# Kernel tuning notes

Measured on AMD Instinct MI355X. Metric: run time of the kernel, lower is better.

The kernel has to match this reference:

```python
import jax, jax.numpy as jnp
import numpy as np

DN = ('NCHW', 'OIHW', 'NCHW')


def setup_inputs() -> dict:
    key = jax.random.key(0)
    k1, k2, k3, k4 = jax.random.split(key, 4)
    B, C, H, W = 8, 64, 128, 416
    depth = jax.random.uniform(k1, (B, H, W), dtype=jnp.float32) * 10.0 + 1.0
    feat = jax.random.normal(k2, (B, C, H, W), dtype=jnp.float32)
    w1 = jax.random.normal(k3, (64, C, 3, 3), dtype=jnp.float32) * 0.05
    w2 = jax.random.normal(k4, (144, 64, 1, 1), dtype=jnp.float32) * 0.05
    return {"depth": depth, "feat": feat, "w1": w1, "w2": w2}


def reference(depth, feat, w1, w2):
    B, H, W = depth.shape
    S = 4  # 2 ** scale, scale=2
    # mask predictor: conv3x3 (no bias) -> relu -> conv1x1 (no bias)
    h = jax.lax.conv_general_dilated(feat, w1, (1, 1), ((1, 1), (1, 1)), dimension_numbers=DN)
    h = jax.nn.relu(h)
    mask = jax.lax.conv_general_dilated(h, w2, (1, 1), ((0, 0), (0, 0)), dimension_numbers=DN)
    # [B, 144, H, W] -> [B, 9, S, S, H, W], softmax over the 9 neighbor taps
    mask = mask.reshape(B, 9, S, S, H, W)
    mask = jax.nn.softmax(mask, axis=1)
    # unfold(depth, 3x3, pad=1): 9 shifted views, row-major (ky, kx) like torch
    pad = jnp.pad(depth, ((0, 0), (1, 1), (1, 1)))
    patches = jnp.stack([pad[:, ky:ky + H, kx:kx + W]
                         for ky in range(3) for kx in range(3)], axis=1)  # [B,9,H,W]
    up = jnp.sum(mask * patches[:, :, None, None], axis=1)  # [B,S,S,H,W]
    # pixel-shuffle: permute(0,3,1,4,2) -> [B,H,S,W,S] -> [B,S*H,S*W]
    out = up.transpose(0, 3, 1, 4, 2).reshape(B, S * H, S * W)
    return out
```

## Files before the change

kernel.cpp:

```cpp
#include <hip/hip_runtime.h>


using frag_ab = __attribute__((ext_vector_type(8))) short;
using frag_cd = __attribute__((ext_vector_type(4))) float;
typedef __attribute__((ext_vector_type(8))) unsigned short ushort8;

static __device__ __forceinline__ unsigned short f2bf(float f) {
    unsigned u = __builtin_bit_cast(unsigned, f);
    u += 0x7fff + ((u >> 16) & 1);
    return (unsigned short)(u >> 16);
}

__global__ void prep(const float* __restrict__ w1, const float* __restrict__ w2,
                     unsigned short* __restrict__ w1bf, unsigned short* __restrict__ w2bf,
                     unsigned short* __restrict__ nhwc, int do_pad) {
    int i = blockIdx.x * 256 + threadIdx.x;
    if (i < 36864) {
        int j = i & 7, oc = (i >> 3) & 63, g = i >> 9;
        int q = g & 3, kh = (g >> 2) & 1, tap = g >> 3;
        int ic = kh * 32 + q * 8 + j;
        w1bf[i] = f2bf(w1[(oc * 64 + ic) * 9 + (tap / 3) * 3 + (tap % 3)]);
    }
    if (i < 9216) {
        int j = i & 7, ch = (i >> 3) % 144, g = (i >> 3) / 144;
        int q = g & 3, kh = g >> 2;
        w2bf[i] = f2bf(w2[ch * 64 + (kh * 32 + q * 8 + j)]);
    }
    if (do_pad && i < 69888) {
        int b = i / 8736, rem = i - b * 8736;
        int pos = rem >> 3, pack = rem & 7;
        int row, w;
        if (pos < 836) { row = (pos < 418) ? 0 : 129; w = (pos < 418) ? pos : pos - 418; }
        else           { int t = pos - 836; row = 1 + (t >> 1); w = (t & 1) ? 417 : 0; }
        ushort8 z = {0, 0, 0, 0, 0, 0, 0, 0};
        *(ushort8*)&nhwc[(((size_t)b * 130 + row) * 418 + w) * 64 + pack * 8] = z;
    }
}

__global__ __launch_bounds__(256, 8) void nchw_to_nhwc(const float* __restrict__ feat,
                                                       unsigned short* __restrict__ nhwc) {
    __shared__ unsigned short sT[32 * 64];
    const int b = blockIdx.z, h = blockIdx.y, w0 = blockIdx.x * 32;
    const int tid = threadIdx.x;
    const int c = tid >> 2, j = tid & 3;
    const float* src = feat + (((size_t)b * 64 + c) * 128 + h) * 416 + w0 + j * 8;
    float4 v0 = *(const float4*)src;
    float4 v1 = *(const float4*)(src + 4);
    sT[(j * 8 + 0) * 64 + c] = f2bf(v0.x);
    sT[(j * 8 + 1) * 64 + c] = f2bf(v0.y);
    sT[(j * 8 + 2) * 64 + c] = f2bf(v0.z);
    sT[(j * 8 + 3) * 64 + c] = f2bf(v0.w);
    sT[(j * 8 + 4) * 64 + c] = f2bf(v1.x);
    sT[(j * 8 + 5) * 64 + c] = f2bf(v1.y);
    sT[(j * 8 + 6) * 64 + c] = f2bf(v1.z);
    sT[(j * 8 + 7) * 64 + c] = f2bf(v1.w);
    __syncthreads();
    const int w = tid >> 3, pack = tid & 7;
    ushort8 val = *(ushort8*)&sT[w * 64 + pack * 8];
    *(ushort8*)&nhwc[(((size_t)b * 130 + h + 1) * 418 + (w0 + w + 1)) * 64 + pack * 8] = val;
}

__global__ __launch_bounds__(256, 4) void convex_up_mfma2(
    const float* __restrict__ depth, const unsigned short* __restrict__ nhwc,
    const unsigned short* __restrict__ w1bf, const unsigned short* __restrict__ w2bf,
    float* __restrict__ out)
{
    constexpr int H = 128, W = 416, OW = 1664;
    constexpr int RS = 418 * 64;

    __shared__ __align__(16) unsigned short sF[1440 * 8];
    __shared__ float sD[180];

    const int tid  = threadIdx.x;
    const int wv   = tid >> 6;
    const int lane = tid & 63;
    const int q    = lane >> 4;
    const int ln   = lane & 15;
    const int bw = blockIdx.x, bh = blockIdx.y, b = blockIdx.z;
    const int h0 = bh * 8, w0 = bw * 16;

    if (tid < 180) {
        int lr = tid / 18, lc = tid % 18;
        int gh = h0 - 1 + lr, gw = w0 - 1 + lc;
        float v = 0.f;
        if ((unsigned)gh < (unsigned)H && (unsigned)gw < (unsigned)W)
            v = depth[((size_t)b * H + gh) * W + gw];
        sD[tid] = v;
    }

    const unsigned short* gbase = nhwc + ((size_t)(b * 130 + h0) * 418 + w0) * 64;
    #pragma unroll
    for (int k = 0; k < 6; ++k) {
        int i = wv + 4 * k;
        int c = i * 64 + lane;
        if (c < 1440) {
            int r = c / 144, m = c - r * 144;
            int col = m >> 3, iccs = m & 7;
            int icc = iccs ^ (col & 7);
            const unsigned short* g = gbase + (size_t)r * RS + col * 64 + icc * 8;
            __builtin_amdgcn_global_load_lds((const __attribute__((address_space(1))) void*)g,
                                             (__attribute__((address_space(3))) void*)&sF[c * 8],
                                             16, 0, 0);
        }
    }
    __syncthreads();

    frag_cd acc1[2][4];
    #pragma unroll
    for (int mt = 0; mt < 2; ++mt)
        #pragma unroll
        for (int nt = 0; nt < 4; ++nt) acc1[mt][nt] = frag_cd{0.f, 0.f, 0.f, 0.f};

    #pragma unroll
    for (int tap = 0; tap < 9; ++tap) {
        const int ky = tap / 3, kx = tap % 3;
        #pragma unroll
        for (int kh = 0; kh < 2; ++kh) {
            frag_ab a[2];
            #pragma unroll
            for (int mt = 0; mt < 2; ++mt) {
                int r = 2 * wv + mt + ky, col = ln + kx;
                int slot = (r * 18 + col) * 8 + ((kh * 4 + q) ^ (col & 7));
                a[mt] = *(const frag_ab*)&sF[slot * 8];
            }
            frag_ab bf[4];
            #pragma unroll
            for (int nt = 0; nt < 4; ++nt)
                bf[nt] = *(const frag_ab*)&w1bf[(size_t)((tap * 2 + kh) * 4 + q) * 512 + (nt * 16 + ln) * 8];
            #pragma unroll
            for (int mt = 0; mt < 2; ++mt)
                #pragma unroll
                for (int nt = 0; nt < 4; ++nt)
                    acc1[mt][nt] = __builtin_amdgcn_mfma_f32_16x16x32_bf16(a[mt], bf[nt], acc1[mt][nt], 0, 0, 0);
        }
    }

    __syncthreads();

    unsigned short* sH = sF + wv * 2304;
    #pragma unroll
    for (int mt = 0; mt < 2; ++mt)
        #pragma unroll
        for (int nt = 0; nt < 4; ++nt)
            #pragma unroll
            for (int r = 0; r < 4; ++r)
                sH[(mt * 16 + q * 4 + r) * 72 + nt * 16 + ln] = f2bf(fmaxf(acc1[mt][nt][r], 0.f));

    frag_cd acc2[2][9];
    #pragma unroll
    for (int mt = 0; mt < 2; ++mt)
        #pragma unroll
        for (int nt = 0; nt < 9; ++nt) acc2[mt][nt] = frag_cd{0.f, 0.f, 0.f, 0.f};

    #pragma unroll
    for (int kh = 0; kh < 2; ++kh) {
        frag_ab a2[2];
        #pragma unroll
        for (int mt = 0; mt < 2; ++mt)
            a2[mt] = *(const frag_ab*)&sH[(mt * 16 + ln) * 72 + kh * 32 + q * 8];
        #pragma unroll
        for (int nt = 0; nt < 9; ++nt) {
            frag_ab b2 = *(const frag_ab*)&w2bf[(size_t)((kh * 4 + q) * 144 + nt * 16 + ln) * 8];
            acc2[0][nt] = __builtin_amdgcn_mfma_f32_16x16x32_bf16(a2[0], b2, acc2[0][nt], 0, 0, 0);
            acc2[1][nt] = __builtin_amdgcn_mfma_f32_16x16x32_bf16(a2[1], b2, acc2[1][nt], 0, 0, 0);
        }
    }

    float* sOutw = (float*)sH;
    #pragma unroll
    for (int mt = 0; mt < 2; ++mt) {
        const int prow = 2 * wv + mt;
        #pragma unroll
        for (int r = 0; r < 4; ++r) {
            const int pcol = q * 4 + r;
            float lg[9];
            #pragma unroll
            for (int t = 0; t < 9; ++t) lg[t] = acc2[mt][t][r];
            float mx = lg[0];
            #pragma unroll
            for (int t = 1; t < 9; ++t) mx = fmaxf(mx, lg[t]);
            float sum = 0.f, up = 0.f;
            #pragma unroll
            for (int t = 0; t < 9; ++t) {
                float e = __expf(lg[t] - mx);
                sum += e;
                up  += e * sD[(prow + t / 3) * 18 + (pcol + t % 3)];
            }
            sOutw[(mt * 16 + pcol) * 17 + ln] = up / sum;
        }
    }
    float* outb = out + (size_t)b * 512 * OW + (size_t)(h0 + 2 * wv) * 4 * OW + w0 * 4;
    const int row_o = lane >> 3;
    const int mt_o  = row_o >> 2, sy_o = row_o & 3;
    #pragma unroll
    for (int v = 0; v < 2; ++v) {
        float4 o;
        #pragma unroll
        for (int e = 0; e < 4; ++e) {
            int j = (lane & 7) * 8 + v * 4 + e;
            o[e] = sOutw[(mt_o * 16 + (j >> 2)) * 17 + sy_o * 4 + (j & 3)];
        }
        *(float4*)&outb[(size_t)row_o * OW + (lane & 7) * 8 + v * 4] = o;
    }
}

__global__ __launch_bounds__(256, 3) void convex_up_mfma_fb(
    const float* __restrict__ depth, const float* __restrict__ feat,
    const unsigned short* __restrict__ w1bf, const unsigned short* __restrict__ w2bf,
    float* __restrict__ out)
{
    constexpr int H = 128, W = 416, OW = 1664;
    __shared__ unsigned short sF[8 * 10 * 18 * 8];
    __shared__ unsigned short sH[4][32 * 72];
    __shared__ float sD[10 * 18];
    const int tid = threadIdx.x, wv = tid >> 6, lane = tid & 63;
    const int q = lane >> 4, ln = lane & 15;
    const int bw = blockIdx.x, bh = blockIdx.y, b = blockIdx.z;
    const int h0 = bh * 8, w0 = bw * 16;
    if (tid < 180) {
        int lr = tid / 18, lc = tid % 18;
        int gh = h0 - 1 + lr, gw = w0 - 1 + lc;
        float v = 0.f;
        if ((unsigned)gh < (unsigned)H && (unsigned)gw < (unsigned)W)
            v = depth[((size_t)b * H + gh) * W + gw];
        sD[tid] = v;
    }
    for (int idx = tid; idx < 11520; idx += 256) {
        int ic = idx / 180, rem = idx - ic * 180;
        int lr = rem / 18, lc = rem - lr * 18;
        int gh = h0 - 1 + lr, gw = w0 - 1 + lc;
        float v = 0.f;
        if ((unsigned)gh < (unsigned)H && (unsigned)gw < (unsigned)W)
            v = feat[(((size_t)b * 64 + ic) * H + gh) * W + gw];
        sF[(((ic >> 3) * 10 + lr) * 18 + lc) * 8 + (ic & 7)] = f2bf(v);
    }
    __syncthreads();
    frag_cd acc1[2][4];
    for (int mt = 0; mt < 2; ++mt) for (int nt = 0; nt < 4; ++nt) acc1[mt][nt] = frag_cd{0.f,0.f,0.f,0.f};
    #pragma unroll
    for (int tap = 0; tap < 9; ++tap) {
        const int ky = tap / 3, kx = tap % 3;
        #pragma unroll
        for (int kh = 0; kh < 2; ++kh) {
            frag_ab a[2];
            #pragma unroll
            for (int mt = 0; mt < 2; ++mt)
                a[mt] = *(const frag_ab*)&sF[(((kh * 4 + q) * 10 + 2 * wv + mt + ky) * 18 + ln + kx) * 8];
            frag_ab bf[4];
            #pragma unroll
            for (int nt = 0; nt < 4; ++nt)
                bf[nt] = *(const frag_ab*)&w1bf[(size_t)((tap * 2 + kh) * 4 + q) * 512 + (nt * 16 + ln) * 8];
            #pragma unroll
            for (int mt = 0; mt < 2; ++mt)
                #pragma unroll
                for (int nt = 0; nt < 4; ++nt)
                    acc1[mt][nt] = __builtin_amdgcn_mfma_f32_16x16x32_bf16(a[mt], bf[nt], acc1[mt][nt], 0, 0, 0);
        }
    }
    #pragma unroll
    for (int mt = 0; mt < 2; ++mt)
        #pragma unroll
        for (int nt = 0; nt < 4; ++nt)
            #pragma unroll
            for (int r = 0; r < 4; ++r)
                sH[wv][(mt * 16 + q * 4 + r) * 72 + nt * 16 + ln] = f2bf(fmaxf(acc1[mt][nt][r], 0.f));
    frag_cd acc2[2][9];
    for (int mt = 0; mt < 2; ++mt) for (int nt = 0; nt < 9; ++nt) acc2[mt][nt] = frag_cd{0.f,0.f,0.f,0.f};
    #pragma unroll
    for (int kh = 0; kh < 2; ++kh) {
        frag_ab a2[2];
        #pragma unroll
        for (int mt = 0; mt < 2; ++mt)
            a2[mt] = *(const frag_ab*)&sH[wv][(mt * 16 + ln) * 72 + kh * 32 + q * 8];
        #pragma unroll
        for (int nt = 0; nt < 9; ++nt) {
            frag_ab b2 = *(const frag_ab*)&w2bf[(size_t)((kh * 4 + q) * 144 + nt * 16 + ln) * 8];
            acc2[0][nt] = __builtin_amdgcn_mfma_f32_16x16x32_bf16(a2[0], b2, acc2[0][nt], 0, 0, 0);
            acc2[1][nt] = __builtin_amdgcn_mfma_f32_16x16x32_bf16(a2[1], b2, acc2[1][nt], 0, 0, 0);
        }
    }
    float* sOutw = (float*)&sH[wv][0];
    #pragma unroll
    for (int mt = 0; mt < 2; ++mt) {
        const int prow = 2 * wv + mt;
        #pragma unroll
        for (int r = 0; r < 4; ++r) {
            const int pcol = q * 4 + r;
            float lg[9];
            #pragma unroll
            for (int t = 0; t < 9; ++t) lg[t] = acc2[mt][t][r];
            float mx = lg[0];
            #pragma unroll
            for (int t = 1; t < 9; ++t) mx = fmaxf(mx, lg[t]);
            float sum = 0.f, up = 0.f;
            #pragma unroll
            for (int t = 0; t < 9; ++t) {
                float e = __expf(lg[t] - mx);
                sum += e; up += e * sD[(prow + t / 3) * 18 + (pcol + t % 3)];
            }
            sOutw[(mt * 16 + pcol) * 17 + ln] = up / sum;
        }
    }
    float* outb = out + (size_t)b * 512 * OW + (size_t)(h0 + 2 * wv) * 4 * OW + w0 * 4;
    const int row_o = lane >> 3, mt_o = row_o >> 2, sy_o = row_o & 3;
    #pragma unroll
    for (int v = 0; v < 2; ++v) {
        float4 o;
        #pragma unroll
        for (int e = 0; e < 4; ++e) {
            int j = (lane & 7) * 8 + v * 4 + e;
            o[e] = sOutw[(mt_o * 16 + (j >> 2)) * 17 + sy_o * 4 + (j & 3)];
        }
        *(float4*)&outb[(size_t)row_o * OW + (lane & 7) * 8 + v * 4] = o;
    }
}

extern "C" void kernel_launch(void* const* d_in, const int* in_sizes, int n_in,
                              void* d_out, int out_size, void* d_ws, size_t ws_size,
                              hipStream_t stream) {
    const float* depth = (const float*)d_in[0];
    const float* feat  = (const float*)d_in[1];
    const float* w1    = (const float*)d_in[2];
    const float* w2    = (const float*)d_in[3];
    float* out = (float*)d_out;

    const size_t NHWC_USHORTS = (size_t)8 * 130 * 418 * 64;
    const size_t NEED = NHWC_USHORTS * 2 + (36864 + 9216) * 2;

    if (ws_size >= NEED) {
        unsigned short* nhwc = (unsigned short*)d_ws;
        unsigned short* w1bf = nhwc + NHWC_USHORTS;
        unsigned short* w2bf = w1bf + 36864;
        prep<<<273, 256, 0, stream>>>(w1, w2, w1bf, w2bf, nhwc, 1);
        nchw_to_nhwc<<<dim3(13, 128, 8), 256, 0, stream>>>(feat, nhwc);
        convex_up_mfma2<<<dim3(26, 16, 8), dim3(256), 0, stream>>>(depth, nhwc, w1bf, w2bf, out);
    } else {
        unsigned short* w1bf = (unsigned short*)d_ws;
        unsigned short* w2bf = w1bf + 36864;
        prep<<<273, 256, 0, stream>>>(w1, w2, w1bf, w2bf, nullptr, 0);
        convex_up_mfma_fb<<<dim3(26, 16, 8), dim3(256), 0, stream>>>(depth, feat, w1bf, w2bf, out);
    }
}
```

Baseline: 241.2 us.

## Widen conv tile to 32 columns, prefetch weights, fold prep into transpose

The fused conv/softmax/upsample kernel now handles a 8x32 pixel tile per block instead of 8x16, so each B-fragment of the 3x3 weights loaded from global memory feeds twice as many MFMAs. The w1 fragments are double-buffered in registers across the 18 k-steps, and the first load is issued before the barrier. The separate weight-conversion and padding prep kernel is merged into the NCHW-to-NHWC transpose kernel, which removes one launch. The cost is a larger shared-memory tile and more accumulator registers, so the launch bound drops to 3 blocks per SM and the grid is halved.

```diff
diff --git a/kernel.cpp b/kernel.cpp
--- a/kernel.cpp
+++ b/kernel.cpp
@@ -37,8 +37,12 @@
     }
 }
 
-__global__ __launch_bounds__(256, 8) void nchw_to_nhwc(const float* __restrict__ feat,
-                                                       unsigned short* __restrict__ nhwc) {
+__global__ __launch_bounds__(256, 8) void nchw_prep(const float* __restrict__ feat,
+                                                    const float* __restrict__ w1,
+                                                    const float* __restrict__ w2,
+                                                    unsigned short* __restrict__ nhwc,
+                                                    unsigned short* __restrict__ w1bf,
+                                                    unsigned short* __restrict__ w2bf) {
     __shared__ unsigned short sT[32 * 64];
     const int b = blockIdx.z, h = blockIdx.y, w0 = blockIdx.x * 32;
     const int tid = threadIdx.x;
@@ -58,9 +62,33 @@
     const int w = tid >> 3, pack = tid & 7;
     ushort8 val = *(ushort8*)&sT[w * 64 + pack * 8];
     *(ushort8*)&nhwc[(((size_t)b * 130 + h + 1) * 418 + (w0 + w + 1)) * 64 + pack * 8] = val;
-}
-
-__global__ __launch_bounds__(256, 4) void convex_up_mfma2(
+
+    if (blockIdx.y == 0) {
+        const int gid = (b * 13 + blockIdx.x) * 256 + tid;
+        for (int i = gid; i < 36864; i += 26624) {
+            int jj = i & 7, oc = (i >> 3) & 63, g = i >> 9;
+            int qq = g & 3, kh = (g >> 2) & 1, tap = g >> 3;
+            int ic = kh * 32 + qq * 8 + jj;
+            w1bf[i] = f2bf(w1[(oc * 64 + ic) * 9 + (tap / 3) * 3 + (tap % 3)]);
+        }
+        if (gid < 9216) {
+            int jj = gid & 7, ch = (gid >> 3) % 144, g = (gid >> 3) / 144;
+            int qq = g & 3, kh = g >> 2;
+            w2bf[gid] = f2bf(w2[ch * 64 + (kh * 32 + qq * 8 + jj)]);
+        }
+        for (int i = gid; i < 69888; i += 26624) {
+            int bb = i / 8736, rem = i - bb * 8736;
+            int pos = rem >> 3, pk = rem & 7;
+            int row, ww;
+            if (pos < 836) { row = (pos < 418) ? 0 : 129; ww = (pos < 418) ? pos : pos - 418; }
+            else           { int t = pos - 836; row = 1 + (t >> 1); ww = (t & 1) ? 417 : 0; }
+            ushort8 z = {0, 0, 0, 0, 0, 0, 0, 0};
+            *(ushort8*)&nhwc[(((size_t)bb * 130 + row) * 418 + ww) * 64 + pk * 8] = z;
+        }
+    }
+}
+
+__global__ __launch_bounds__(256, 3) void convex_up_mfma3(
     const float* __restrict__ depth, const unsigned short* __restrict__ nhwc,
     const unsigned short* __restrict__ w1bf, const unsigned short* __restrict__ w2bf,
     float* __restrict__ out)
@@ -68,8 +96,8 @@
     constexpr int H = 128, W = 416, OW = 1664;
     constexpr int RS = 418 * 64;
 
-    __shared__ __align__(16) unsigned short sF[1440 * 8];
-    __shared__ float sD[180];
+    __shared__ __align__(16) unsigned short sF[2720 * 8];
+    __shared__ float sD[340];
 
     const int tid  = threadIdx.x;
     const int wv   = tid >> 6;
@@ -77,24 +105,24 @@
     const int q    = lane >> 4;
     const int ln   = lane & 15;
     const int bw = blockIdx.x, bh = blockIdx.y, b = blockIdx.z;
-    const int h0 = bh * 8, w0 = bw * 16;
-
-    if (tid < 180) {
-        int lr = tid / 18, lc = tid % 18;
+    const int h0 = bh * 8, w0 = bw * 32;
+
+    for (int t = tid; t < 340; t += 256) {
+        int lr = t / 34, lc = t - lr * 34;
         int gh = h0 - 1 + lr, gw = w0 - 1 + lc;
         float v = 0.f;
         if ((unsigned)gh < (unsigned)H && (unsigned)gw < (unsigned)W)
             v = depth[((size_t)b * H + gh) * W + gw];
-        sD[tid] = v;
+        sD[t] = v;
     }
 
     const unsigned short* gbase = nhwc + ((size_t)(b * 130 + h0) * 418 + w0) * 64;
     #pragma unroll
-    for (int k = 0; k < 6; ++k) {
+    for (int k = 0; k < 11; ++k) {
         int i = wv + 4 * k;
         int c = i * 64 + lane;
-        if (c < 1440) {
-            int r = c / 144, m = c - r * 144;
+        if (c < 2720) {
+            int r = c / 272, m = c - r * 272;
             int col = m >> 3, iccs = m & 7;
             int icc = iccs ^ (col & 7);
             const unsigned short* g = gbase + (size_t)r * RS + col * 64 + icc * 8;
@@ -103,104 +131,125 @@
                                              16, 0, 0);
         }
     }
+
+    frag_cd acc1[2][2][4];
+    #pragma unroll
+    for (int hf = 0; hf < 2; ++hf)
+        #pragma unroll
+        for (int mt = 0; mt < 2; ++mt)
+            #pragma unroll
+            for (int nt = 0; nt < 4; ++nt) acc1[hf][mt][nt] = frag_cd{0.f, 0.f, 0.f, 0.f};
+
+    frag_ab bfp[2][4];
+    #pragma unroll
+    for (int nt = 0; nt < 4; ++nt)
+        bfp[0][nt] = *(const frag_ab*)&w1bf[(size_t)q * 512 + (nt * 16 + ln) * 8];
+
     __syncthreads();
 
-    frag_cd acc1[2][4];
-    #pragma unroll
-    for (int mt = 0; mt < 2; ++mt)
-        #pragma unroll
-        for (int nt = 0; nt < 4; ++nt) acc1[mt][nt] = frag_cd{0.f, 0.f, 0.f, 0.f};
-
-    #pragma unroll
-    for (int tap = 0; tap < 9; ++tap) {
+    #pragma unroll
+    for (int s = 0; s < 18; ++s) {
+        const int tap = s >> 1, kh = s & 1;
         const int ky = tap / 3, kx = tap % 3;
-        #pragma unroll
-        for (int kh = 0; kh < 2; ++kh) {
+        if (s < 17) {
+            #pragma unroll
+            for (int nt = 0; nt < 4; ++nt)
+                bfp[(s + 1) & 1][nt] =
+                    *(const frag_ab*)&w1bf[(size_t)((s + 1) * 4 + q) * 512 + (nt * 16 + ln) * 8];
+        }
+        #pragma unroll
+        for (int hf = 0; hf < 2; ++hf) {
             frag_ab a[2];
             #pragma unroll
             for (int mt = 0; mt < 2; ++mt) {
-                int r = 2 * wv + mt + ky, col = ln + kx;
-                int slot = (r * 18 + col) * 8 + ((kh * 4 + q) ^ (col & 7));
+                int r = 2 * wv + mt + ky, col = ln + kx + 16 * hf;
+                int slot = (r * 34 + col) * 8 + ((kh * 4 + q) ^ (col & 7));
                 a[mt] = *(const frag_ab*)&sF[slot * 8];
             }
-            frag_ab bf[4];
+            #pragma unroll
+            for (int mt = 0; mt < 2; ++mt)
+                #pragma unroll
+                for (int nt = 0; nt < 4; ++nt)
+                    acc1[hf][mt][nt] = __builtin_amdgcn_mfma_f32_16x16x32_bf16(
+                        a[mt], bfp[s & 1][nt], acc1[hf][mt][nt], 0, 0, 0);
+        }
+    }
+
+    __syncthreads();
+
+    unsigned short* sH = sF + wv * 4608;
+    #pragma unroll
+    for (int hf = 0; hf < 2; ++hf)
+        #pragma unroll
+        for (int mt = 0; mt < 2; ++mt)
             #pragma unroll
             for (int nt = 0; nt < 4; ++nt)
-                bf[nt] = *(const frag_ab*)&w1bf[(size_t)((tap * 2 + kh) * 4 + q) * 512 + (nt * 16 + ln) * 8];
-            #pragma unroll
-            for (int mt = 0; mt < 2; ++mt)
-                #pragma unroll
-                for (int nt = 0; nt < 4; ++nt)
-                    acc1[mt][nt] = __builtin_amdgcn_mfma_f32_16x16x32_bf16(a[mt], bf[nt], acc1[mt][nt], 0, 0, 0);
-        }
-    }
-
-    __syncthreads();
-
-    unsigned short* sH = sF + wv * 2304;
-    #pragma unroll
-    for (int mt = 0; mt < 2; ++mt)
-        #pragma unroll
-        for (int nt = 0; nt < 4; ++nt)
-            #pragma unroll
-            for (int r = 0; r < 4; ++r)
-                sH[(mt * 16 + q * 4 + r) * 72 + nt * 16 + ln] = f2bf(fmaxf(acc1[mt][nt][r], 0.f));
-
-    frag_cd acc2[2][9];
-    #pragma unroll
-    for (int mt = 0; mt < 2; ++mt)
-        #pragma unroll
-        for (int nt = 0; nt < 9; ++nt) acc2[mt][nt] = frag_cd{0.f, 0.f, 0.f, 0.f};
-
-    #pragma unroll
-    for (int kh = 0; kh < 2; ++kh) {
-        frag_ab a2[2];
-        #pragma unroll
-        for (int mt = 0; mt < 2; ++mt)
-            a2[mt] = *(const frag_ab*)&sH[(mt * 16 + ln) * 72 + kh * 32 + q * 8];
-        #pragma unroll
-        for (int nt = 0; nt < 9; ++nt) {
-            frag_ab b2 = *(const frag_ab*)&w2bf[(size_t)((kh * 4 + q) * 144 + nt * 16 + ln) * 8];
-            acc2[0][nt] = __builtin_amdgcn_mfma_f32_16x16x32_bf16(a2[0], b2, acc2[0][nt], 0, 0, 0);
-            acc2[1][nt] = __builtin_amdgcn_mfma_f32_16x16x32_bf16(a2[1], b2, acc2[1][nt], 0, 0, 0);
-        }
-    }
+                #pragma unroll
+                for (int r = 0; r < 4; ++r)
+                    sH[(hf * 32 + mt * 16 + q * 4 + r) * 72 + nt * 16 + ln] =
+                        f2bf(fmaxf(acc1[hf][mt][nt][r], 0.f));
 
     float* sOutw = (float*)sH;
-    #pragma unroll
-    for (int mt = 0; mt < 2; ++mt) {
-        const int prow = 2 * wv + mt;
-        #pragma unroll
-        for (int r = 0; r < 4; ++r) {
-            const int pcol = q * 4 + r;
-            float lg[9];
-            #pragma unroll
-            for (int t = 0; t < 9; ++t) lg[t] = acc2[mt][t][r];
-            float mx = lg[0];
-            #pragma unroll
-            for (int t = 1; t < 9; ++t) mx = fmaxf(mx, lg[t]);
-            float sum = 0.f, up = 0.f;
-            #pragma unroll
-            for (int t = 0; t < 9; ++t) {
-                float e = __expf(lg[t] - mx);
-                sum += e;
-                up  += e * sD[(prow + t / 3) * 18 + (pcol + t % 3)];
-            }
-            sOutw[(mt * 16 + pcol) * 17 + ln] = up / sum;
-        }
-    }
-    float* outb = out + (size_t)b * 512 * OW + (size_t)(h0 + 2 * wv) * 4 * OW + w0 * 4;
     const int row_o = lane >> 3;
     const int mt_o  = row_o >> 2, sy_o = row_o & 3;
-    #pragma unroll
-    for (int v = 0; v < 2; ++v) {
-        float4 o;
-        #pragma unroll
-        for (int e = 0; e < 4; ++e) {
-            int j = (lane & 7) * 8 + v * 4 + e;
-            o[e] = sOutw[(mt_o * 16 + (j >> 2)) * 17 + sy_o * 4 + (j & 3)];
-        }
-        *(float4*)&outb[(size_t)row_o * OW + (lane & 7) * 8 + v * 4] = o;
+
+    #pragma unroll
+    for (int hf = 0; hf < 2; ++hf) {
+        frag_cd acc2[2][9];
+        #pragma unroll
+        for (int mt = 0; mt < 2; ++mt)
+            #pragma unroll
+            for (int nt = 0; nt < 9; ++nt) acc2[mt][nt] = frag_cd{0.f, 0.f, 0.f, 0.f};
+
+        #pragma unroll
+        for (int kh = 0; kh < 2; ++kh) {
+            frag_ab a2[2];
+            #pragma unroll
+            for (int mt = 0; mt < 2; ++mt)
+                a2[mt] = *(const frag_ab*)&sH[(hf * 32 + mt * 16 + ln) * 72 + kh * 32 + q * 8];
+            #pragma unroll
+            for (int nt = 0; nt < 9; ++nt) {
+                frag_ab b2 = *(const frag_ab*)&w2bf[(size_t)((kh * 4 + q) * 144 + nt * 16 + ln) * 8];
+                acc2[0][nt] = __builtin_amdgcn_mfma_f32_16x16x32_bf16(a2[0], b2, acc2[0][nt], 0, 0, 0);
+                acc2[1][nt] = __builtin_amdgcn_mfma_f32_16x16x32_bf16(a2[1], b2, acc2[1][nt], 0, 0, 0);
+            }
+        }
+
+        #pragma unroll
+        for (int mt = 0; mt < 2; ++mt) {
+            const int prow = 2 * wv + mt;
+            #pragma unroll
+            for (int r = 0; r < 4; ++r) {
+                const int pcol = q * 4 + r;
+                const int dcol = hf * 16 + pcol;
+                float lg[9];
+                #pragma unroll
+                for (int t = 0; t < 9; ++t) lg[t] = acc2[mt][t][r];
+                float mx = lg[0];
+                #pragma unroll
+                for (int t = 1; t < 9; ++t) mx = fmaxf(mx, lg[t]);
+                float sum = 0.f, up = 0.f;
+                #pragma unroll
+                for (int t = 0; t < 9; ++t) {
+                    float e = __expf(lg[t] - mx);
+                    sum += e;
+                    up  += e * sD[(prow + t / 3) * 34 + (dcol + t % 3)];
+                }
+                sOutw[(mt * 16 + pcol) * 17 + ln] = up / sum;
+            }
+        }
+        float* outb = out + (size_t)b * 512 * OW + (size_t)(h0 + 2 * wv) * 4 * OW
+                    + (size_t)(w0 + hf * 16) * 4;
+        #pragma unroll
+        for (int v = 0; v < 2; ++v) {
+            float4 o;
+            #pragma unroll
+            for (int e = 0; e < 4; ++e) {
+                int j = (lane & 7) * 8 + v * 4 + e;
+                o[e] = sOutw[(mt_o * 16 + (j >> 2)) * 17 + sy_o * 4 + (j & 3)];
+            }
+            *(float4*)&outb[(size_t)row_o * OW + (lane & 7) * 8 + v * 4] = o;
+        }
     }
 }
 
@@ -331,13 +380,12 @@
         unsigned short* nhwc = (unsigned short*)d_ws;
         unsigned short* w1bf = nhwc + NHWC_USHORTS;
         unsigned short* w2bf = w1bf + 36864;
-        prep<<<273, 256, 0, stream>>>(w1, w2, w1bf, w2bf, nhwc, 1);
-        nchw_to_nhwc<<<dim3(13, 128, 8), 256, 0, stream>>>(feat, nhwc);
-        convex_up_mfma2<<<dim3(26, 16, 8), dim3(256), 0, stream>>>(depth, nhwc, w1bf, w2bf, out);
+        nchw_prep<<<dim3(13, 128, 8), 256, 0, stream>>>(feat, w1, w2, nhwc, w1bf, w2bf);
+        convex_up_mfma3<<<dim3(13, 16, 8), dim3(256), 0, stream>>>(depth, nhwc, w1bf, w2bf, out);
     } else {
         unsigned short* w1bf = (unsigned short*)d_ws;
         unsigned short* w2bf = w1bf + 36864;
         prep<<<273, 256, 0, stream>>>(w1, w2, w1bf, w2bf, nullptr, 0);
-        convex_up_mfma_fb<<<dim3(26, 16, 8), dim3(256), 0, stream>>>(depth, feat, w1bf, w2bf, out);
-    }
-}
+        convex_up_mfma_fb<<<dim3(26, 16, 8), 256, 0, stream>>>(depth, feat, w1bf, w2bf, out);
+    }
+}
```

After: 249.7 us. +3.5%, slower.
